# Optimization experiments

Measured on AMD Instinct MI355X. Metric: run time of the kernel, lower is better.

Reference implementation:

```python
import jax, jax.numpy as jnp
import numpy as np

# Config (DiffWave-style)
C = 64        # channels
K = 3         # kernel_size
L = 30        # num_layers
CYCLES = 3    # num_cycles
DRATE = 2     # dilation_rate
ITER = 50     # diffusion steps
ESIZE = 128   # embedding_size
EPROJ = 512   # embedding_proj
EFACT = 4.0   # embedding_factor
B, T = 4, 16384
LAYERS_PER_CYCLE = L // CYCLES
DILATIONS = [DRATE ** (i % LAYERS_PER_CYCLE) for i in range(L)]
INV_SQRT2 = 1.0 / np.sqrt(2.0).astype(np.float32)


def _embed_table():
    # [ITER, ESIZE] sinusoidal noise-schedule embedding (deterministic buffer)
    logit = jnp.linspace(0.0, 1.0, ESIZE // 2)
    exp = jnp.power(10.0, logit * EFACT)
    t = jnp.arange(1, ITER + 1, dtype=jnp.float32)
    comp = exp[None, :] * t[:, None]
    return jnp.concatenate([jnp.sin(comp), jnp.cos(comp)], axis=-1)


def _dconv(x, w, d):
    # x: [B,T,Cin], w: [K,Cin,Cout], SAME padding, dilation d -> [B,T,Cout]
    return jax.lax.conv_general_dilated(
        x, w, window_strides=(1,), padding='SAME', rhs_dilation=(d,),
        dimension_numbers=('NWC', 'WIO', 'NWC'))


def setup_inputs() -> dict:
    key = jax.random.key(0)
    ks = jax.random.split(key, 20)
    g = lambda k, shape, fan_in: (jax.random.normal(k, shape) / np.sqrt(fan_in)).astype(jnp.float32)
    return {
        'signal': jax.random.normal(ks[0], (B, T), dtype=jnp.float32),
        'timestep': jax.random.randint(ks[1], (B,), 1, ITER + 1, dtype=jnp.int32),
        'in_w': g(ks[2], (1, C), 1),
        'in_b': jnp.zeros((C,), jnp.float32),
        'pe0_w': g(ks[3], (ESIZE, EPROJ), ESIZE),
        'pe0_b': jnp.zeros((EPROJ,), jnp.float32),
        'pe1_w': g(ks[4], (EPROJ, EPROJ), EPROJ),
        'pe1_b': jnp.zeros((EPROJ,), jnp.float32),
        'blk_emb_w': g(ks[5], (L, EPROJ, C), EPROJ),
        'blk_emb_b': jnp.zeros((L, C), jnp.float32),
        'blk_conv_w': g(ks[6], (L, K, C, 2 * C), K * C),
        'blk_conv_b': jnp.zeros((L, 2 * C), jnp.float32),
        'blk_res_w': g(ks[7], (L - 1, C, C), C),
        'blk_res_b': jnp.zeros((L - 1, C), jnp.float32),
        'blk_skip_w': g(ks[8], (L, C, C), C),
        'blk_skip_b': jnp.zeros((L, C), jnp.float32),
        'out0_w': g(ks[9], (C, C), C),
        'out0_b': jnp.zeros((C,), jnp.float32),
        'out1_w': g(ks[10], (C, 1), C),
        'out1_b': jnp.zeros((1,), jnp.float32),
    }


def reference(signal, timestep, in_w, in_b, pe0_w, pe0_b, pe1_w, pe1_b,
              blk_emb_w, blk_emb_b, blk_conv_w, blk_conv_b,
              blk_res_w, blk_res_b, blk_skip_w, blk_skip_b,
              out0_w, out0_b, out1_w, out1_b):
    # input 1x1 conv + relu: [B,T] -> [B,T,C]
    x = jax.nn.relu(signal[..., None] * in_w[0][None, None, :] + in_b)
    # noise-schedule embedding [B,ESIZE] -> swish MLP -> [B,EPROJ]
    embed = _embed_table()[timestep - 1]
    embed = jax.nn.swish(embed @ pe0_w + pe0_b)
    embed = jax.nn.swish(embed @ pe1_w + pe1_b)
    skip_sum = jnp.zeros_like(x)
    for i in range(L):
        e = embed @ blk_emb_w[i] + blk_emb_b[i]           # [B,C]
        h = x + e[:, None, :]                              # [B,T,C]
        y = _dconv(h, blk_conv_w[i], DILATIONS[i]) + blk_conv_b[i]  # [B,T,2C]
        z = jnp.tanh(y[..., :C]) * jax.nn.sigmoid(y[..., C:])       # gated
        if i < L - 1:
            x = (z @ blk_res_w[i] + blk_res_b[i] + x) * INV_SQRT2
        skip_sum = skip_sum + (z @ blk_skip_w[i] + blk_skip_b[i])
    ctx = skip_sum / np.sqrt(L).astype(np.float32)
    ctx = jax.nn.relu(ctx @ out0_w + out0_b)
    out = ctx @ out1_w + out1_b                            # [B,T,1]
    return jnp.squeeze(out, axis=-1)
```

## Files before the change

### kernel.cpp

```cpp
#include <hip/hip_runtime.h>
#include <math.h>

#define TT 16384
#define BB 4
#define CC 64
#define LL 30

typedef _Float16 f16;
typedef _Float16 f16x4 __attribute__((ext_vector_type(4)));
typedef _Float16 f16x8 __attribute__((ext_vector_type(8)));
typedef float f32x4 __attribute__((ext_vector_type(4)));
typedef unsigned int u32;

#define MFMA(a, b, c) __builtin_amdgcn_mfma_f32_16x16x32_f16(a, b, c, 0, 0, 0)

__device__ __forceinline__ float fsig(float x) { return 1.0f / (1.0f + __expf(-x)); }
__device__ __forceinline__ float ftanhf(float x) { return 1.0f - 2.0f / (__expf(2.0f * x) + 1.0f); }

__device__ __forceinline__ void gl_lds16(const void* g, void* l) {
    __builtin_amdgcn_global_load_lds((const __attribute__((address_space(1))) u32*)g,
                                     (__attribute__((address_space(3))) u32*)l, 16, 0, 0);
}

__global__ void pack_weights(const float* __restrict__ conv_w, const float* __restrict__ res_w,
                             const float* __restrict__ skip_w, const float* __restrict__ out0_w,
                             f16* __restrict__ wcv, f16* __restrict__ wrs, f16* __restrict__ wsk,
                             f16* __restrict__ wo0) {
    const int total_c = LL * 6 * 8 * 64 * 8;
    const int total_r = (LL - 1) * 2 * 4 * 64 * 8;
    const int total_s = LL * 2 * 4 * 64 * 8;
    const int total_o = 2 * 4 * 64 * 8;
    const int total = total_c + total_r + total_s + total_o;
    for (int i = blockIdx.x * blockDim.x + threadIdx.x; i < total; i += gridDim.x * blockDim.x) {
        if (i < total_c) {
            int e = i & 7, lane = (i >> 3) & 63, mf = (i >> 9) & 7, rest = i >> 12;
            int ks = rest % 6, l = rest / 6;
            int cin = (ks & 1) * 32 + (lane >> 4) * 8 + e;
            int tap = ks >> 1;
            int cout = mf * 16 + (lane & 15);
            wcv[i] = (f16)conv_w[(((size_t)l * 3 + tap) * 64 + cin) * 128 + cout];
        } else if (i < total_c + total_r) {
            int j = i - total_c;
            int e = j & 7, lane = (j >> 3) & 63, mf = (j >> 9) & 3, kk = (j >> 11) & 1, l = j >> 12;
            int cin = kk * 32 + (lane >> 4) * 8 + e;
            int cout = mf * 16 + (lane & 15);
            wrs[j] = (f16)res_w[((size_t)l * 64 + cin) * 64 + cout];
        } else if (i < total_c + total_r + total_s) {
            int j = i - total_c - total_r;
            int e = j & 7, lane = (j >> 3) & 63, mf = (j >> 9) & 3, kk = (j >> 11) & 1, l = j >> 12;
            int cin = kk * 32 + (lane >> 4) * 8 + e;
            int cout = mf * 16 + (lane & 15);
            wsk[j] = (f16)skip_w[((size_t)l * 64 + cin) * 64 + cout];
        } else {
            int j = i - total_c - total_r - total_s;
            int e = j & 7, lane = (j >> 3) & 63, mf = (j >> 9) & 3, kk = (j >> 11) & 1;
            int cin = kk * 32 + (lane >> 4) * 8 + e;
            int c = mf * 16 + (lane & 15);
            wo0[j] = (f16)out0_w[cin * 64 + c];
        }
    }
}

__global__ void init_x_kernel(const float* __restrict__ signal, const float* __restrict__ in_w,
                              const float* __restrict__ in_b, f16* __restrict__ x0) {
    int i = blockIdx.x * 256 + threadIdx.x;
    int bt = i >> 3, g = i & 7;
    float s = signal[bt];
    f32x4 w0 = *(const f32x4*)&in_w[g * 8];
    f32x4 w1 = *(const f32x4*)&in_w[g * 8 + 4];
    f32x4 b0 = *(const f32x4*)&in_b[g * 8];
    f32x4 b1 = *(const f32x4*)&in_b[g * 8 + 4];
    f16x8 o;
#pragma unroll
    for (int j = 0; j < 4; ++j) {
        o[j] = (f16)fmaxf(s * w0[j] + b0[j], 0.f);
        o[4 + j] = (f16)fmaxf(s * w1[j] + b1[j], 0.f);
    }
    *(f16x8*)&x0[(size_t)bt * CC + g * 8] = o;
}

__global__ void embed_stage1(const int* __restrict__ timestep, const float* __restrict__ pe0_w,
                             const float* __restrict__ pe0_b, float* __restrict__ h1) {
    __shared__ float emb[BB * 128];
    const int tid = threadIdx.x;
    for (int i = tid; i < BB * 128; i += 256) {
        int b = i >> 7, j = i & 127, jj = j & 63;
        float logit = (jj == 63) ? 1.0f : (float)jj * (1.0f / 63.0f);
        double e10 = pow(10.0, (double)(4.0f * logit));
        float comp = (float)e10 * (float)timestep[b];
        emb[i] = (j < 64) ? (float)sin((double)comp) : (float)cos((double)comp);
    }
    __syncthreads();
    const int col = blockIdx.x * 64 + (tid & 63), b = tid >> 6;
    float s = 0.f;
    for (int j = 0; j < 128; ++j) s += emb[b * 128 + j] * pe0_w[j * 512 + col];
    s += pe0_b[col];
    h1[b * 512 + col] = s * fsig(s);
}

__global__ void embed_stage2(const float* __restrict__ h1, const float* __restrict__ pe1_w,
                             const float* __restrict__ pe1_b, float* __restrict__ embed2) {
    __shared__ float hs[BB * 512];
    const int tid = threadIdx.x;
    for (int i = tid; i < BB * 512; i += 256) hs[i] = h1[i];
    __syncthreads();
    const int col = blockIdx.x * 64 + (tid & 63), b = tid >> 6;
    float s = 0.f;
    for (int j = 0; j < 512; ++j) s += hs[b * 512 + j] * pe1_w[j * 512 + col];
    s += pe1_b[col];
    embed2[b * 512 + col] = s * fsig(s);
}

__global__ void e_kernel(const float* __restrict__ embed2, const float* __restrict__ blk_emb_w,
                         const float* __restrict__ blk_emb_b, float* __restrict__ e_out) {
    const int l = blockIdx.x, b = blockIdx.y;
    const int tid = threadIdx.x;
    __shared__ float em[512];
    __shared__ float red[256];
    for (int i = tid; i < 512; i += 256) em[i] = embed2[b * 512 + i];
    __syncthreads();
    const int c = tid & 63, part = tid >> 6;
    float s0 = 0.f, s1 = 0.f;
    for (int j = part * 128; j < part * 128 + 128; j += 2) {
        s0 += em[j] * blk_emb_w[((size_t)l * 512 + j) * 64 + c];
        s1 += em[j + 1] * blk_emb_w[((size_t)l * 512 + j + 1) * 64 + c];
    }
    red[tid] = s0 + s1;
    __syncthreads();
    if (tid < 64)
        e_out[(l * BB + b) * 64 + tid] =
            red[tid] + red[tid + 64] + red[tid + 128] + red[tid + 192] + blk_emb_b[l * 64 + tid];
}

__global__ void evec2_kernel(const float* __restrict__ e_in, const float* __restrict__ conv_w,
                             const float* __restrict__ conv_b, float* __restrict__ evec) {
    const int l = blockIdx.x, tap = blockIdx.y, b = blockIdx.z;
    const int n = threadIdx.x;
    __shared__ float es[64];
    if (n < 64) es[n] = e_in[(l * BB + b) * 64 + n];
    __syncthreads();
    const float* cw = conv_w + ((size_t)(l * 3 + tap) * 64) * 128;
    float a0 = 0.f, a1 = 0.f, a2 = 0.f, a3 = 0.f;
#pragma unroll
    for (int k = 0; k < 64; k += 4) {
        a0 += es[k] * cw[k * 128 + n];
        a1 += es[k + 1] * cw[(k + 1) * 128 + n];
        a2 += es[k + 2] * cw[(k + 2) * 128 + n];
        a3 += es[k + 3] * cw[(k + 3) * 128 + n];
    }
    float s = a0 + a1 + a2 + a3 + ((tap == 1) ? conv_b[l * 128 + n] : 0.f);
    evec[((size_t)(l * 4 + b) * 3 + tap) * 128 + n] = s;
}

__global__ void sbsum_kernel(const float* __restrict__ skip_b, float* __restrict__ sbsum) {
    int c = threadIdx.x;
    float s = 0.f;
    for (int l = 0; l < LL; ++l) s += skip_b[l * 64 + c];
    sbsum[c] = s;
}

__launch_bounds__(256)
__global__ void layer_kernel(const f16* __restrict__ xin, f16* __restrict__ xout,
                             f16* __restrict__ zg,
                             const f16* __restrict__ wcv, const f16* __restrict__ wrs,
                             const float* __restrict__ evec_l, const float* __restrict__ res_b,
                             const f16* __restrict__ zpage, int d) {
    __shared__ f16 xs[3 * 64 * 64];
    __shared__ f16 zs[64 * 64];
    const int tid = threadIdx.x, lane = tid & 63, w = tid >> 6;
    const int lrow = lane & 15, lk = lane >> 4;
    const int b = blockIdx.y, t0 = blockIdx.x * 64;
    const f16* xb = xin + (size_t)b * TT * CC;
    f16* zb = zg + (size_t)b * TT * CC;

#pragma unroll
    for (int j = 0; j < 6; ++j) {
        int chunk = j * 4 + w;
        int gid = chunk * 64 + lane;
        int tap = gid >> 9, row = (gid >> 3) & 63, g = gid & 7;
        int t = t0 + row + (tap - 1) * d;
        const f16* src = ((unsigned)t < TT) ? (xb + (size_t)t * CC + ((g ^ (row & 7)) << 3)) : zpage;
        gl_lds16(src, (void*)((char*)xs + chunk * 1024));
    }
    __syncthreads();

    f32x4 acc[2][4] = {};
#pragma unroll
    for (int ks = 0; ks < 6; ++ks) {
        const int tap = ks >> 1, kk = ks & 1;
        f16x8 aw0 = *(const f16x8*)&wcv[((ks * 8 + w) * 64 + lane) * 8];
        f16x8 aw1 = *(const f16x8*)&wcv[((ks * 8 + w + 4) * 64 + lane) * 8];
#pragma unroll
        for (int nfi = 0; nfi < 4; ++nfi) {
            int trow = nfi * 16 + lrow;
            int r = tap * 64 + trow;
            int g = kk * 4 + lk;
            f16x8 bx = *(const f16x8*)&xs[r * 64 + ((g ^ (r & 7)) << 3)];
            acc[0][nfi] = MFMA(aw0, bx, acc[0][nfi]);
            acc[1][nfi] = MFMA(aw1, bx, acc[1][nfi]);
        }
    }

    const float* evb = evec_l + b * 384;
    const int ca = w * 16 + lk * 4;
    const int gz = ca >> 3;
    f32x4 e0a = *(const f32x4*)&evb[ca], e1a = *(const f32x4*)&evb[128 + ca],
          e2a = *(const f32x4*)&evb[256 + ca];
    f32x4 e0b = *(const f32x4*)&evb[64 + ca], e1b = *(const f32x4*)&evb[192 + ca],
          e2b = *(const f32x4*)&evb[320 + ca];
#pragma unroll
    for (int nfi = 0; nfi < 4; ++nfi) {
        int trow = nfi * 16 + lrow;
        int t = t0 + trow;
        float m0 = (t >= d) ? 1.f : 0.f;
        float m2 = (t + d < TT) ? 1.f : 0.f;
        f16x4 zo;
#pragma unroll
        for (int r = 0; r < 4; ++r) {
            float ya = acc[0][nfi][r] + e1a[r] + m0 * e0a[r] + m2 * e2a[r];
            float yb = acc[1][nfi][r] + e1b[r] + m0 * e0b[r] + m2 * e2b[r];
            zo[r] = (f16)(ftanhf(ya) * fsig(yb));
        }
        *(f16x4*)&zs[trow * 64 + ((gz ^ (trow & 7)) << 3) + (ca & 7)] = zo;
        *(f16x4*)&zb[(size_t)(t0 + trow) * CC + ca] = zo;
    }

    if (wrs != nullptr) {
        __syncthreads();
        f32x4 accR[4] = {};
#pragma unroll
        for (int kk = 0; kk < 2; ++kk) {
            f16x8 ar_ = *(const f16x8*)&wrs[((kk * 4 + w) * 64 + lane) * 8];
#pragma unroll
            for (int nfi = 0; nfi < 4; ++nfi) {
                int trow = nfi * 16 + lrow;
                int g = kk * 4 + lk;
                f16x8 bz = *(const f16x8*)&zs[trow * 64 + ((g ^ (trow & 7)) << 3)];
                accR[nfi] = MFMA(ar_, bz, accR[nfi]);
            }
        }
        f16* xob = xout + (size_t)b * TT * CC;
        f32x4 rb4 = *(const f32x4*)&res_b[ca];
#pragma unroll
        for (int nfi = 0; nfi < 4; ++nfi) {
            int trow = nfi * 16 + lrow;
            int rr = 64 + trow;
            f16x4 xv = *(const f16x4*)&xs[rr * 64 + ((gz ^ (rr & 7)) << 3) + (ca & 7)];
            f16x4 xo;
#pragma unroll
            for (int r = 0; r < 4; ++r)
                xo[r] = (f16)((accR[nfi][r] + rb4[r] + (float)xv[r]) * 0.70710678118654752f);
            *(f16x4*)&xob[(size_t)(t0 + trow) * CC + ca] = xo;
        }
    }
}

__launch_bounds__(256)
__global__ void skip_head(const f16* __restrict__ zbuf, const f16* __restrict__ z29,
                          const f16* __restrict__ wsk, const f16* __restrict__ wo0,
                          const float* __restrict__ sbsum, const float* __restrict__ out0_b,
                          const float* __restrict__ out1_w, const float* __restrict__ out1_b,
                          float* __restrict__ out) {
    __shared__ float red[64 * 65];
    const int tid = threadIdx.x, lane = tid & 63, w = tid >> 6;
    const int lrow = lane & 15, lk = lane >> 4;
    const int lin = blockIdx.x;
    const int lin2 = (lin & 7) * 128 + (lin >> 3);
    const int b = lin2 >> 8, tile = lin2 & 255;
    const int t0 = tile * 64;

#define ZL(L) ((((L) < LL - 1) ? (zbuf + (size_t)(L) * BB * TT * CC) : z29) + \
               ((size_t)b * TT + t0) * CC)
#define ZLOAD(DST, ZP)                                                           \
    _Pragma("unroll") for (int nt = 0; nt < 4; ++nt) _Pragma("unroll")           \
        for (int kk = 0; kk < 2; ++kk) {                                         \
        DST[nt * 2 + kk] =                                                       \
            *(const f16x8*)((ZP) + ((size_t)(nt * 16 + lrow)) * CC + kk * 32 + lk * 8); \
    }

    f32x4 accS[4][4] = {};
    f16x8 zr[2][8];
    {
        const f16* zp0 = ZL(w);
        ZLOAD(zr[0], zp0);
    }
#pragma unroll
    for (int li = 0; li < 8; ++li) {
        const int l = w + li * 4;
        if (l < LL) {
            if (l + 4 < LL) {
                const f16* zpn = ZL(l + 4);
                ZLOAD(zr[(li + 1) & 1], zpn);
            }
            const f16* wl = wsk + (size_t)l * 4096;
#pragma unroll
            for (int kk = 0; kk < 2; ++kk) {
#pragma unroll
                for (int mf = 0; mf < 4; ++mf) {
                    f16x8 as_ = *(const f16x8*)&wl[((kk * 4 + mf) * 64 + lane) * 8];
#pragma unroll
                    for (int nt = 0; nt < 4; ++nt)
                        accS[mf][nt] = MFMA(as_, zr[li & 1][nt * 2 + kk], accS[mf][nt]);
                }
            }
        }
    }
#undef ZLOAD
#undef ZL

    __syncthreads();
#pragma unroll
    for (int ph = 0; ph < 4; ++ph) {
        if (w == ph) {
#pragma unroll
            for (int mf = 0; mf < 4; ++mf) {
#pragma unroll
                for (int nt = 0; nt < 4; ++nt) {
                    int row = nt * 16 + lrow;
                    int base = row * 65 + mf * 16 + lk * 4;
#pragma unroll
                    for (int r = 0; r < 4; ++r) {
                        if (ph == 0) red[base + r] = accS[mf][nt][r];
                        else red[base + r] += accS[mf][nt][r];
                    }
                }
            }
        }
        __syncthreads();
    }

    const float invL = 0.18257418583505537f;
    const int trow = w * 16 + lrow;
    f32x4 accO[4] = {};
#pragma unroll
    for (int kk = 0; kk < 2; ++kk) {
        const int ch0 = kk * 32 + lk * 8;
        f32x4 sb0 = *(const f32x4*)&sbsum[ch0];
        f32x4 sb1 = *(const f32x4*)&sbsum[ch0 + 4];
        f16x8 bz;
#pragma unroll
        for (int j = 0; j < 4; ++j) {
            bz[j] = (f16)((red[trow * 65 + ch0 + j] + sb0[j]) * invL);
            bz[4 + j] = (f16)((red[trow * 65 + ch0 + 4 + j] + sb1[j]) * invL);
        }
#pragma unroll
        for (int mf = 0; mf < 4; ++mf) {
            f16x8 aw = *(const f16x8*)&wo0[((kk * 4 + mf) * 64 + lane) * 8];
            accO[mf] = MFMA(aw, bz, accO[mf]);
        }
    }
    float pv = 0.f;
    const float b1 = out1_b[0];
#pragma unroll
    for (int mf = 0; mf < 4; ++mf) {
        int c = mf * 16 + lk * 4;
        f32x4 b0 = *(const f32x4*)&out0_b[c];
        f32x4 w1 = *(const f32x4*)&out1_w[c];
#pragma unroll
        for (int r = 0; r < 4; ++r) pv += fmaxf(accO[mf][r] + b0[r], 0.f) * w1[r];
    }
    pv += __shfl_xor(pv, 16);
    pv += __shfl_xor(pv, 32);
    if (lane < 16) out[(size_t)b * TT + t0 + w * 16 + lane] = pv + b1;
}

extern "C" void kernel_launch(void* const* d_in, const int* in_sizes, int n_in,
                              void* d_out, int out_size, void* d_ws, size_t ws_size,
                              hipStream_t stream) {
    const float* signal = (const float*)d_in[0];
    const int* timestep = (const int*)d_in[1];
    const float* in_w = (const float*)d_in[2];
    const float* in_b = (const float*)d_in[3];
    const float* pe0_w = (const float*)d_in[4];
    const float* pe0_b = (const float*)d_in[5];
    const float* pe1_w = (const float*)d_in[6];
    const float* pe1_b = (const float*)d_in[7];
    const float* blk_emb_w = (const float*)d_in[8];
    const float* blk_emb_b = (const float*)d_in[9];
    const float* blk_conv_w = (const float*)d_in[10];
    const float* blk_conv_b = (const float*)d_in[11];
    const float* blk_res_w = (const float*)d_in[12];
    const float* blk_res_b = (const float*)d_in[13];
    const float* blk_skip_w = (const float*)d_in[14];
    const float* blk_skip_b = (const float*)d_in[15];
    const float* out0_w = (const float*)d_in[16];
    const float* out0_b = (const float*)d_in[17];
    const float* out1_w = (const float*)d_in[18];
    const float* out1_b = (const float*)d_in[19];

    char* p = (char*)d_ws;
    const size_t xhsz = (size_t)BB * TT * CC * sizeof(f16);
    const size_t BTC = (size_t)BB * TT * CC;
    f16* xa = (f16*)p; p += xhsz;
    f16* xb2 = (f16*)p; p += xhsz;
    f16* wcv = (f16*)p; p += (size_t)737280 * 2;
    f16* wrs = (f16*)p; p += (size_t)118784 * 2;
    f16* wsk = (f16*)p; p += (size_t)122880 * 2;
    f16* wo0 = (f16*)p; p += (size_t)4096 * 2;
    float* h1 = (float*)p; p += 4 * 512 * sizeof(float);
    float* embed2 = (float*)p; p += 4 * 512 * sizeof(float);
    float* e_buf = (float*)p; p += (size_t)LL * BB * 64 * sizeof(float);
    float* evec = (float*)p; p += (size_t)LL * 4 * 3 * 128 * sizeof(float);
    float* sbsum = (float*)p; p += 64 * sizeof(float);
    f16* zpage = (f16*)p; p += 256;
    p = (char*)(((size_t)p + 255) & ~(size_t)255);
    f16* zbuf = (f16*)p; p += (size_t)(LL - 1) * xhsz;

    hipMemsetAsync(zpage, 0, 256, stream);
    pack_weights<<<1024, 256, 0, stream>>>(blk_conv_w, blk_res_w, blk_skip_w, out0_w,
                                           wcv, wrs, wsk, wo0);
    init_x_kernel<<<2048, 256, 0, stream>>>(signal, in_w, in_b, xa);
    embed_stage1<<<8, 256, 0, stream>>>(timestep, pe0_w, pe0_b, h1);
    embed_stage2<<<8, 256, 0, stream>>>(h1, pe1_w, pe1_b, embed2);
    e_kernel<<<dim3(LL, BB), 256, 0, stream>>>(embed2, blk_emb_w, blk_emb_b, e_buf);
    evec2_kernel<<<dim3(LL, 3, BB), 128, 0, stream>>>(e_buf, blk_conv_w, blk_conv_b, evec);
    sbsum_kernel<<<1, 64, 0, stream>>>(blk_skip_b, sbsum);

    f16* cur = xa;
    f16* nxt = xb2;
    f16* z29 = xa;
    for (int i = 0; i < LL; ++i) {
        int d = 1 << (i % 10);
        bool last = (i == LL - 1);
        f16* zg = last ? nxt : (zbuf + (size_t)i * BTC);
        if (last) z29 = nxt;
        layer_kernel<<<dim3(TT / 64, BB), 256, 0, stream>>>(
            cur, nxt, zg, wcv + (size_t)i * 24576,
            last ? nullptr : (wrs + (size_t)i * 4096), evec + (size_t)i * 1536,
            last ? nullptr : (blk_res_b + i * 64), zpage, d);
        if (!last) { f16* t = cur; cur = nxt; nxt = t; }
    }

    skip_head<<<(BB * TT) / 64, 256, 0, stream>>>(zbuf, z29, wsk, wo0, sbsum, out0_b, out1_w,
                                                  out1_b, (float*)d_out);
}
```

Measured before the change: 565.7 us.

## Repartition layer MFMA work by time rows per wave and halve skip_head tile

```diff
diff --git a/kernel.cpp b/kernel.cpp
--- a/kernel.cpp
+++ b/kernel.cpp
@@ -184,73 +184,70 @@
     }
     __syncthreads();
 
-    f32x4 acc[2][4] = {};
+    const int trow = w * 16 + lrow;
+    const int tglob = t0 + trow;
+
+    f32x4 acc[8] = {};
 #pragma unroll
     for (int ks = 0; ks < 6; ++ks) {
         const int tap = ks >> 1, kk = ks & 1;
-        f16x8 aw0 = *(const f16x8*)&wcv[((ks * 8 + w) * 64 + lane) * 8];
-        f16x8 aw1 = *(const f16x8*)&wcv[((ks * 8 + w + 4) * 64 + lane) * 8];
-#pragma unroll
-        for (int nfi = 0; nfi < 4; ++nfi) {
-            int trow = nfi * 16 + lrow;
-            int r = tap * 64 + trow;
+        int r = tap * 64 + trow;
+        int g = kk * 4 + lk;
+        f16x8 bx = *(const f16x8*)&xs[r * 64 + ((g ^ (r & 7)) << 3)];
+#pragma unroll
+        for (int mf = 0; mf < 8; ++mf) {
+            f16x8 aw = *(const f16x8*)&wcv[((ks * 8 + mf) * 64 + lane) * 8];
+            acc[mf] = MFMA(aw, bx, acc[mf]);
+        }
+    }
+
+    const float* evb = evec_l + b * 384;
+    const float m0 = (tglob >= d) ? 1.f : 0.f;
+    const float m2 = (tglob + d < TT) ? 1.f : 0.f;
+#pragma unroll
+    for (int mf = 0; mf < 4; ++mf) {
+        const int cb = mf * 16 + lk * 4;
+        f32x4 e0a = *(const f32x4*)&evb[cb], e1a = *(const f32x4*)&evb[128 + cb],
+              e2a = *(const f32x4*)&evb[256 + cb];
+        f32x4 e0b = *(const f32x4*)&evb[64 + cb], e1b = *(const f32x4*)&evb[192 + cb],
+              e2b = *(const f32x4*)&evb[320 + cb];
+        f16x4 zo;
+#pragma unroll
+        for (int r = 0; r < 4; ++r) {
+            float ya = acc[mf][r] + e1a[r] + m0 * e0a[r] + m2 * e2a[r];
+            float yb = acc[mf + 4][r] + e1b[r] + m0 * e0b[r] + m2 * e2b[r];
+            zo[r] = (f16)(ftanhf(ya) * fsig(yb));
+        }
+        const int g2 = cb >> 3;
+        *(f16x4*)&zs[trow * 64 + ((g2 ^ (trow & 7)) << 3) + (cb & 7)] = zo;
+        *(f16x4*)&zb[(size_t)tglob * CC + cb] = zo;
+    }
+
+    if (wrs != nullptr) {
+        f32x4 accR[4] = {};
+#pragma unroll
+        for (int kk = 0; kk < 2; ++kk) {
             int g = kk * 4 + lk;
-            f16x8 bx = *(const f16x8*)&xs[r * 64 + ((g ^ (r & 7)) << 3)];
-            acc[0][nfi] = MFMA(aw0, bx, acc[0][nfi]);
-            acc[1][nfi] = MFMA(aw1, bx, acc[1][nfi]);
-        }
-    }
-
-    const float* evb = evec_l + b * 384;
-    const int ca = w * 16 + lk * 4;
-    const int gz = ca >> 3;
-    f32x4 e0a = *(const f32x4*)&evb[ca], e1a = *(const f32x4*)&evb[128 + ca],
-          e2a = *(const f32x4*)&evb[256 + ca];
-    f32x4 e0b = *(const f32x4*)&evb[64 + ca], e1b = *(const f32x4*)&evb[192 + ca],
-          e2b = *(const f32x4*)&evb[320 + ca];
-#pragma unroll
-    for (int nfi = 0; nfi < 4; ++nfi) {
-        int trow = nfi * 16 + lrow;
-        int t = t0 + trow;
-        float m0 = (t >= d) ? 1.f : 0.f;
-        float m2 = (t + d < TT) ? 1.f : 0.f;
-        f16x4 zo;
-#pragma unroll
-        for (int r = 0; r < 4; ++r) {
-            float ya = acc[0][nfi][r] + e1a[r] + m0 * e0a[r] + m2 * e2a[r];
-            float yb = acc[1][nfi][r] + e1b[r] + m0 * e0b[r] + m2 * e2b[r];
-            zo[r] = (f16)(ftanhf(ya) * fsig(yb));
-        }
-        *(f16x4*)&zs[trow * 64 + ((gz ^ (trow & 7)) << 3) + (ca & 7)] = zo;
-        *(f16x4*)&zb[(size_t)(t0 + trow) * CC + ca] = zo;
-    }
-
-    if (wrs != nullptr) {
-        __syncthreads();
-        f32x4 accR[4] = {};
-#pragma unroll
-        for (int kk = 0; kk < 2; ++kk) {
-            f16x8 ar_ = *(const f16x8*)&wrs[((kk * 4 + w) * 64 + lane) * 8];
-#pragma unroll
-            for (int nfi = 0; nfi < 4; ++nfi) {
-                int trow = nfi * 16 + lrow;
-                int g = kk * 4 + lk;
-                f16x8 bz = *(const f16x8*)&zs[trow * 64 + ((g ^ (trow & 7)) << 3)];
-                accR[nfi] = MFMA(ar_, bz, accR[nfi]);
+            f16x8 bz = *(const f16x8*)&zs[trow * 64 + ((g ^ (trow & 7)) << 3)];
+#pragma unroll
+            for (int mf = 0; mf < 4; ++mf) {
+                f16x8 ar_ = *(const f16x8*)&wrs[((kk * 4 + mf) * 64 + lane) * 8];
+                accR[mf] = MFMA(ar_, bz, accR[mf]);
             }
         }
         f16* xob = xout + (size_t)b * TT * CC;
-        f32x4 rb4 = *(const f32x4*)&res_b[ca];
-#pragma unroll
-        for (int nfi = 0; nfi < 4; ++nfi) {
-            int trow = nfi * 16 + lrow;
-            int rr = 64 + trow;
-            f16x4 xv = *(const f16x4*)&xs[rr * 64 + ((gz ^ (rr & 7)) << 3) + (ca & 7)];
+        const int rr = 64 + trow;
+#pragma unroll
+        for (int mf = 0; mf < 4; ++mf) {
+            const int cb = mf * 16 + lk * 4;
+            f32x4 rb4 = *(const f32x4*)&res_b[cb];
+            const int gx = cb >> 3;
+            f16x4 xv = *(const f16x4*)&xs[rr * 64 + ((gx ^ (rr & 7)) << 3) + (cb & 7)];
             f16x4 xo;
 #pragma unroll
             for (int r = 0; r < 4; ++r)
-                xo[r] = (f16)((accR[nfi][r] + rb4[r] + (float)xv[r]) * 0.70710678118654752f);
-            *(f16x4*)&xob[(size_t)(t0 + trow) * CC + ca] = xo;
+                xo[r] = (f16)((accR[mf][r] + rb4[r] + (float)xv[r]) * 0.70710678118654752f);
+            *(f16x4*)&xob[(size_t)tglob * CC + cb] = xo;
         }
     }
 }
@@ -261,25 +258,25 @@
                           const float* __restrict__ sbsum, const float* __restrict__ out0_b,
                           const float* __restrict__ out1_w, const float* __restrict__ out1_b,
                           float* __restrict__ out) {
-    __shared__ float red[64 * 65];
+    __shared__ float red[32 * 65];
     const int tid = threadIdx.x, lane = tid & 63, w = tid >> 6;
     const int lrow = lane & 15, lk = lane >> 4;
     const int lin = blockIdx.x;
-    const int lin2 = (lin & 7) * 128 + (lin >> 3);
-    const int b = lin2 >> 8, tile = lin2 & 255;
-    const int t0 = tile * 64;
+    const int lin2 = (lin & 7) * 256 + (lin >> 3);
+    const int b = lin2 >> 9, tile = lin2 & 511;
+    const int t0 = tile * 32;
 
 #define ZL(L) ((((L) < LL - 1) ? (zbuf + (size_t)(L) * BB * TT * CC) : z29) + \
                ((size_t)b * TT + t0) * CC)
-#define ZLOAD(DST, ZP)                                                           \
-    _Pragma("unroll") for (int nt = 0; nt < 4; ++nt) _Pragma("unroll")           \
-        for (int kk = 0; kk < 2; ++kk) {                                         \
-        DST[nt * 2 + kk] =                                                       \
+#define ZLOAD(DST, ZP)                                                                  \
+    _Pragma("unroll") for (int nt = 0; nt < 2; ++nt) _Pragma("unroll")                  \
+        for (int kk = 0; kk < 2; ++kk) {                                                \
+        DST[nt * 2 + kk] =                                                              \
             *(const f16x8*)((ZP) + ((size_t)(nt * 16 + lrow)) * CC + kk * 32 + lk * 8); \
     }
 
-    f32x4 accS[4][4] = {};
-    f16x8 zr[2][8];
+    f32x4 accS[4][2] = {};
+    f16x8 zr[2][4];
     {
         const f16* zp0 = ZL(w);
         ZLOAD(zr[0], zp0);
@@ -299,7 +296,7 @@
                 for (int mf = 0; mf < 4; ++mf) {
                     f16x8 as_ = *(const f16x8*)&wl[((kk * 4 + mf) * 64 + lane) * 8];
 #pragma unroll
-                    for (int nt = 0; nt < 4; ++nt)
+                    for (int nt = 0; nt < 2; ++nt)
                         accS[mf][nt] = MFMA(as_, zr[li & 1][nt * 2 + kk], accS[mf][nt]);
                 }
             }
@@ -315,7 +312,7 @@
 #pragma unroll
             for (int mf = 0; mf < 4; ++mf) {
 #pragma unroll
-                for (int nt = 0; nt < 4; ++nt) {
+                for (int nt = 0; nt < 2; ++nt) {
                     int row = nt * 16 + lrow;
                     int base = row * 65 + mf * 16 + lk * 4;
 #pragma unroll
@@ -329,39 +326,41 @@
         __syncthreads();
     }
 
-    const float invL = 0.18257418583505537f;
-    const int trow = w * 16 + lrow;
-    f32x4 accO[4] = {};
-#pragma unroll
-    for (int kk = 0; kk < 2; ++kk) {
-        const int ch0 = kk * 32 + lk * 8;
-        f32x4 sb0 = *(const f32x4*)&sbsum[ch0];
-        f32x4 sb1 = *(const f32x4*)&sbsum[ch0 + 4];
-        f16x8 bz;
-#pragma unroll
-        for (int j = 0; j < 4; ++j) {
-            bz[j] = (f16)((red[trow * 65 + ch0 + j] + sb0[j]) * invL);
-            bz[4 + j] = (f16)((red[trow * 65 + ch0 + 4 + j] + sb1[j]) * invL);
-        }
+    if (w < 2) {
+        const float invL = 0.18257418583505537f;
+        const int trow = w * 16 + lrow;
+        f32x4 accO[4] = {};
+#pragma unroll
+        for (int kk = 0; kk < 2; ++kk) {
+            const int ch0 = kk * 32 + lk * 8;
+            f32x4 sb0 = *(const f32x4*)&sbsum[ch0];
+            f32x4 sb1 = *(const f32x4*)&sbsum[ch0 + 4];
+            f16x8 bz;
+#pragma unroll
+            for (int j = 0; j < 4; ++j) {
+                bz[j] = (f16)((red[trow * 65 + ch0 + j] + sb0[j]) * invL);
+                bz[4 + j] = (f16)((red[trow * 65 + ch0 + 4 + j] + sb1[j]) * invL);
+            }
+#pragma unroll
+            for (int mf = 0; mf < 4; ++mf) {
+                f16x8 aw = *(const f16x8*)&wo0[((kk * 4 + mf) * 64 + lane) * 8];
+                accO[mf] = MFMA(aw, bz, accO[mf]);
+            }
+        }
+        float pv = 0.f;
+        const float b1 = out1_b[0];
 #pragma unroll
         for (int mf = 0; mf < 4; ++mf) {
-            f16x8 aw = *(const f16x8*)&wo0[((kk * 4 + mf) * 64 + lane) * 8];
-            accO[mf] = MFMA(aw, bz, accO[mf]);
-        }
-    }
-    float pv = 0.f;
-    const float b1 = out1_b[0];
-#pragma unroll
-    for (int mf = 0; mf < 4; ++mf) {
-        int c = mf * 16 + lk * 4;
-        f32x4 b0 = *(const f32x4*)&out0_b[c];
-        f32x4 w1 = *(const f32x4*)&out1_w[c];
-#pragma unroll
-        for (int r = 0; r < 4; ++r) pv += fmaxf(accO[mf][r] + b0[r], 0.f) * w1[r];
-    }
-    pv += __shfl_xor(pv, 16);
-    pv += __shfl_xor(pv, 32);
-    if (lane < 16) out[(size_t)b * TT + t0 + w * 16 + lane] = pv + b1;
+            int c = mf * 16 + lk * 4;
+            f32x4 b0 = *(const f32x4*)&out0_b[c];
+            f32x4 w1 = *(const f32x4*)&out1_w[c];
+#pragma unroll
+            for (int r = 0; r < 4; ++r) pv += fmaxf(accO[mf][r] + b0[r], 0.f) * w1[r];
+        }
+        pv += __shfl_xor(pv, 16);
+        pv += __shfl_xor(pv, 32);
+        if (lane < 16) out[(size_t)b * TT + t0 + w * 16 + lane] = pv + b1;
+    }
 }
 
 extern "C" void kernel_launch(void* const* d_in, const int* in_sizes, int n_in,
@@ -431,6 +430,6 @@
         if (!last) { f16* t = cur; cur = nxt; nxt = t; }
     }
 
-    skip_head<<<(BB * TT) / 64, 256, 0, stream>>>(zbuf, z29, wsk, wo0, sbsum, out0_b, out1_w,
+    skip_head<<<(BB * TT) / 32, 256, 0, stream>>>(zbuf, z29, wsk, wo0, sbsum, out0_b, out1_w,
                                                   out1_b, (float*)d_out);
 }
```

Result: slower. 707.2 us (+25.0%).
